# Kernel tuning notes

Measured on AMD Instinct MI355X. Metric: run time of the kernel, lower is better.

The kernel has to match this reference:

```python
import jax, jax.numpy as jnp
import numpy as np

B, H, T, D = 2, 16, 2048, 64


def setup_inputs() -> dict:
    key = jax.random.key(0)
    kq, kk, kv, km = jax.random.split(key, 4)
    q = jax.random.normal(kq, (B, H, T, D), dtype=jnp.float32)
    k = jax.random.normal(kk, (B, H, T, D), dtype=jnp.float32)
    v = jax.random.normal(kv, (B, H, T, D), dtype=jnp.float32)
    mask = jax.random.randint(km, (T, T), 0, 2, dtype=jnp.int32)
    return {"q": q, "k": k, "v": v, "mask": mask}


def reference(q, k, v, mask):
    d_k = q.shape[-1]
    scale = jnp.asarray(d_k, q.dtype) ** -0.5
    # (B,H,T,D) @ (B,H,D,T) -> (B,H,T,T)
    scores = jnp.einsum("bhtd,bhsd->bhts", q * scale, k)
    # mask broadcast over (B,H); masked positions set to -1e9 as in torch code
    scores = jnp.where(mask[None, None, :, :] == 0, jnp.asarray(-1e9, scores.dtype), scores)
    attn = jax.nn.softmax(scores, axis=-1)
    # (B,H,T,T) @ (B,H,T,D) -> (B,H,T,D)
    out = jnp.einsum("bhts,bhsd->bhtd", attn, v)
    return (out, attn)
```

## Files before the change

kernel.cpp:

```cpp
#include <hip/hip_runtime.h>
#include <hip/hip_bf16.h>
#include <cstddef>

#define T_SEQ 2048
#define D_HEAD 64
#define BC 64
#define NKT (T_SEQ / BC)
#define PAD 72

typedef __bf16 bf16x8 __attribute__((ext_vector_type(8)));
typedef float f32x4 __attribute__((ext_vector_type(4)));
typedef unsigned short u16x8 __attribute__((ext_vector_type(8)));

__device__ __forceinline__ unsigned short f2bf(float f) {
  __bf16 h = (__bf16)f;
  return __builtin_bit_cast(unsigned short, h);
}
__device__ __forceinline__ bf16x8 ldfrag(const unsigned short* p) {
  u16x8 t = *(const u16x8*)p;
  return __builtin_bit_cast(bf16x8, t);
}
__device__ __forceinline__ f32x4 mfma16(bf16x8 a, bf16x8 b, f32x4 c) {
  return __builtin_amdgcn_mfma_f32_16x16x32_bf16(a, b, c, 0, 0, 0);
}
__device__ __forceinline__ void bar_sync() {
  asm volatile("" ::: "memory");
  __builtin_amdgcn_s_barrier();
  asm volatile("" ::: "memory");
}
__device__ __forceinline__ void lds_fence() {
  asm volatile("s_waitcnt lgkmcnt(0)" ::: "memory");
}
__device__ __forceinline__ float exp2_hw(float x) { return __builtin_amdgcn_exp2f(x); }
__device__ __forceinline__ float log2_hw(float x) { return __builtin_amdgcn_logf(x); }

__global__ __launch_bounds__(256) void mask_pack(const int* __restrict__ maskg,
                                                 unsigned* __restrict__ mp) {
  const size_t total = (size_t)T_SEQ * T_SEQ;
  size_t idx = (size_t)blockIdx.x * blockDim.x + threadIdx.x;
  const size_t stride = (size_t)gridDim.x * blockDim.x;
  const int lane = threadIdx.x & 63;
  for (; idx < total; idx += stride) {
    int mv = maskg[idx];
    unsigned long long b = __ballot(mv != 0);
    if (lane == 0)       mp[idx >> 5] = (unsigned)b;
    else if (lane == 32) mp[idx >> 5] = (unsigned)(b >> 32);
  }
}

__global__ __launch_bounds__(256, 5) void attn_fused2(
    const float* __restrict__ qg, const float* __restrict__ kg,
    const float* __restrict__ vg, const unsigned* __restrict__ mpk,
    float* __restrict__ outg, float* __restrict__ attng)
{
  __shared__ unsigned short ks[BC][PAD];
  __shared__ unsigned short vt[D_HEAD][PAD];
  __shared__ unsigned short ps[64][PAD];

  const int bid = blockIdx.x;
  const int lin = (bid & 7) * 128 + (bid >> 3);
  const int bh  = lin >> 5;
  const int strip = lin & 31;

  const int tid  = threadIdx.x;
  const int lane = tid & 63;
  const int wid  = tid >> 6;
  const int lr = lane & 15, lh = lane >> 4;
  const int r0 = strip * 64 + wid * 16;
  const int sv = tid >> 2;
  const int sc4 = (tid & 3) << 4;
  const int vt7 = tid & 7;
  const int vs2 = (tid >> 3) * 2;

  const float C = 0.18033688011112042f;
  const float* qb = qg + (size_t)bh * T_SEQ * D_HEAD;
  const float* kb = kg + (size_t)bh * T_SEQ * D_HEAD;
  const float* vb = vg + (size_t)bh * T_SEQ * D_HEAD;
  const int ROWW = T_SEQ / 32;

  bf16x8 qf[2];
  {
    const float* qr = qb + (size_t)(r0 + lr) * D_HEAD;
    #pragma unroll
    for (int kk = 0; kk < 2; ++kk) {
      float4 a = *(const float4*)(qr + kk * 32 + lh * 8);
      float4 b = *(const float4*)(qr + kk * 32 + lh * 8 + 4);
      u16x8 u;
      u[0] = f2bf(a.x); u[1] = f2bf(a.y); u[2] = f2bf(a.z); u[3] = f2bf(a.w);
      u[4] = f2bf(b.x); u[5] = f2bf(b.y); u[6] = f2bf(b.z); u[7] = f2bf(b.w);
      qf[kk] = __builtin_bit_cast(bf16x8, u);
    }
  }

  const f32x4 zero4 = {0.f, 0.f, 0.f, 0.f};
  f32x4 acc[4];
  #pragma unroll
  for (int nt = 0; nt < 4; ++nt) acc[nt] = zero4;
  float psum_s = 0.f;

  for (int kt = 0; kt < NKT; ++kt) {
    const int n0 = kt * BC;
    bar_sync();
    {
      const float* ksrc = kb + (size_t)(n0 + sv) * D_HEAD + sc4;
      float4 k0 = *(const float4*)(ksrc + 0),  k1 = *(const float4*)(ksrc + 4);
      float4 k2 = *(const float4*)(ksrc + 8),  k3 = *(const float4*)(ksrc + 12);
      *(ushort4*)&ks[sv][sc4 + 0]  = make_ushort4(f2bf(k0.x), f2bf(k0.y), f2bf(k0.z), f2bf(k0.w));
      *(ushort4*)&ks[sv][sc4 + 4]  = make_ushort4(f2bf(k1.x), f2bf(k1.y), f2bf(k1.z), f2bf(k1.w));
      *(ushort4*)&ks[sv][sc4 + 8]  = make_ushort4(f2bf(k2.x), f2bf(k2.y), f2bf(k2.z), f2bf(k2.w));
      *(ushort4*)&ks[sv][sc4 + 12] = make_ushort4(f2bf(k3.x), f2bf(k3.y), f2bf(k3.z), f2bf(k3.w));
    }
    {
      const float* v0 = vb + (size_t)(n0 + vs2) * D_HEAD + vt7;
      const float* v1 = v0 + D_HEAD;
      #pragma unroll
      for (int j = 0; j < 8; ++j) {
        const float a = v0[8 * j];
        const float b = v1[8 * j];
        const unsigned w = (unsigned)f2bf(a) | ((unsigned)f2bf(b) << 16);
        *(unsigned*)&vt[vt7 + 8 * j][vs2] = w;
      }
    }
    const unsigned mw0 = mpk[(size_t)(r0 + lr) * ROWW + kt * 2];
    const unsigned mw1 = mpk[(size_t)(r0 + lr) * ROWW + kt * 2 + 1];
    lds_fence(); bar_sync();

    f32x4 st[4];
    #pragma unroll
    for (int nt = 0; nt < 4; ++nt) st[nt] = zero4;
    #pragma unroll
    for (int kk = 0; kk < 2; ++kk) {
      bf16x8 kf[4];
      #pragma unroll
      for (int nt = 0; nt < 4; ++nt) kf[nt] = ldfrag(&ks[nt * 16 + lr][kk * 32 + lh * 8]);
      #pragma unroll
      for (int nt = 0; nt < 4; ++nt) st[nt] = mfma16(kf[nt], qf[kk], st[nt]);
    }
    #pragma unroll
    for (int nt = 0; nt < 4; ++nt) {
      const unsigned w = (nt & 2) ? mw1 : mw0;
      float p[4];
      #pragma unroll
      for (int r = 0; r < 4; ++r) {
        const int bit = (nt & 1) * 16 + 4 * lh + r;
        p[r] = ((w >> bit) & 1) ? exp2_hw(st[nt][r] * C) : 0.f;
        psum_s += p[r];
      }
      const unsigned w0 = (unsigned)f2bf(p[0]) | ((unsigned)f2bf(p[1]) << 16);
      const unsigned w1 = (unsigned)f2bf(p[2]) | ((unsigned)f2bf(p[3]) << 16);
      *(unsigned*)&ps[wid * 16 + lr][nt * 16 + 4 * lh]     = w0;
      *(unsigned*)&ps[wid * 16 + lr][nt * 16 + 4 * lh + 2] = w1;
    }
    lds_fence();
    #pragma unroll
    for (int kk = 0; kk < 2; ++kk) {
      const bf16x8 pa = ldfrag(&ps[wid * 16 + lr][kk * 32 + lh * 8]);
      #pragma unroll
      for (int nt = 0; nt < 4; ++nt) {
        const bf16x8 vf = ldfrag(&vt[nt * 16 + lr][kk * 32 + lh * 8]);
        acc[nt] = mfma16(pa, vf, acc[nt]);
      }
    }
  }

  {
    psum_s += __shfl_xor(psum_s, 16);
    psum_s += __shfl_xor(psum_s, 32);
  }
  const float iv_s = 1.0f / psum_s;
  float ivq[4], lg2ivq[4];
  #pragma unroll
  for (int r = 0; r < 4; ++r) {
    ivq[r] = __shfl(iv_s, 4 * lh + r);
    lg2ivq[r] = log2_hw(ivq[r]);
  }

  float* ob = outg + (size_t)(bh * T_SEQ + r0) * D_HEAD;
  #pragma unroll
  for (int nt = 0; nt < 4; ++nt)
    #pragma unroll
    for (int r = 0; r < 4; ++r)
      ob[(size_t)(4 * lh + r) * D_HEAD + nt * 16 + lr] = acc[nt][r] * ivq[r];

  float* ab = attng + (size_t)(bh * T_SEQ + r0) * T_SEQ;
  for (int kt = 0; kt < NKT; ++kt) {
    const int n0 = kt * BC;
    bar_sync();
    {
      const float* ksrc = kb + (size_t)(n0 + sv) * D_HEAD + sc4;
      float4 k0 = *(const float4*)(ksrc + 0),  k1 = *(const float4*)(ksrc + 4);
      float4 k2 = *(const float4*)(ksrc + 8),  k3 = *(const float4*)(ksrc + 12);
      *(ushort4*)&ks[sv][sc4 + 0]  = make_ushort4(f2bf(k0.x), f2bf(k0.y), f2bf(k0.z), f2bf(k0.w));
      *(ushort4*)&ks[sv][sc4 + 4]  = make_ushort4(f2bf(k1.x), f2bf(k1.y), f2bf(k1.z), f2bf(k1.w));
      *(ushort4*)&ks[sv][sc4 + 8]  = make_ushort4(f2bf(k2.x), f2bf(k2.y), f2bf(k2.z), f2bf(k2.w));
      *(ushort4*)&ks[sv][sc4 + 12] = make_ushort4(f2bf(k3.x), f2bf(k3.y), f2bf(k3.z), f2bf(k3.w));
    }
    unsigned mw[4][2];
    #pragma unroll
    for (int r = 0; r < 4; ++r) {
      const size_t mrow = (size_t)(r0 + 4 * lh + r) * ROWW + kt * 2;
      mw[r][0] = mpk[mrow];
      mw[r][1] = mpk[mrow + 1];
    }
    lds_fence(); bar_sync();

    f32x4 sc_[4];
    #pragma unroll
    for (int nt = 0; nt < 4; ++nt) sc_[nt] = zero4;
    #pragma unroll
    for (int kk = 0; kk < 2; ++kk) {
      bf16x8 kf[4];
      #pragma unroll
      for (int nt = 0; nt < 4; ++nt) kf[nt] = ldfrag(&ks[nt * 16 + lr][kk * 32 + lh * 8]);
      #pragma unroll
      for (int nt = 0; nt < 4; ++nt) sc_[nt] = mfma16(qf[kk], kf[nt], sc_[nt]);
    }
    #pragma unroll
    for (int r = 0; r < 4; ++r) {
      float* arow = ab + (size_t)(4 * lh + r) * T_SEQ + n0;
      #pragma unroll
      for (int nt = 0; nt < 4; ++nt) {
        const int mv = (mw[r][nt >> 1] >> ((nt & 1) * 16 + lr)) & 1;
        const float p = mv ? exp2_hw(__builtin_fmaf(sc_[nt][r], C, lg2ivq[r])) : 0.f;
        __builtin_nontemporal_store(p, arow + nt * 16 + lr);
      }
    }
  }
}

__global__ __launch_bounds__(512, 2) void attn_fused_fb(
    const float* __restrict__ qg, const float* __restrict__ kg,
    const float* __restrict__ vg, const int* __restrict__ maskg,
    float* __restrict__ outg, float* __restrict__ attng)
{
  __shared__ unsigned short qs[128][PAD];
  __shared__ unsigned short ks[64][PAD];
  __shared__ unsigned short vt[64][PAD];
  __shared__ unsigned short pp[128][PAD];
  __shared__ float rsum[128];
  int bid = blockIdx.x;
  int lin = (bid & 7) * 64 + (bid >> 3);
  int bh = lin >> 4, br0 = (lin & 15) * 128;
  const int tid = threadIdx.x, lane = tid & 63, wid = tid >> 6;
  const int wm = wid >> 1, wn = wid & 1, lr = lane & 15, lh = lane >> 4;
  const float scale = 0.125f;
  const float* qb = qg + ((size_t)bh * T_SEQ + br0) * D_HEAD;
  const float* kbp = kg + (size_t)bh * T_SEQ * D_HEAD;
  const float* vbp = vg + (size_t)bh * T_SEQ * D_HEAD;
  if (tid < 128) rsum[tid] = 0.f;
  #pragma unroll
  for (int it = 0; it < 4; ++it) {
    int idx = it * 512 + tid;
    int r = idx >> 4, c = (idx & 15) << 2;
    float4 f = *(const float4*)(qb + (size_t)r * D_HEAD + c);
    *(ushort4*)&qs[r][c] = make_ushort4(f2bf(f.x), f2bf(f.y), f2bf(f.z), f2bf(f.w));
  }
  f32x4 acc_o[2][2];
  const f32x4 zero4 = {0.f, 0.f, 0.f, 0.f};
  #pragma unroll
  for (int a = 0; a < 2; ++a)
    #pragma unroll
    for (int b = 0; b < 2; ++b) acc_o[a][b] = zero4;
  float psum[2][4] = {{0.f,0.f,0.f,0.f},{0.f,0.f,0.f,0.f}};
  __syncthreads();
  for (int kt = 0; kt < NKT; ++kt) {
    const int kb0 = kt * 64;
    #pragma unroll
    for (int it = 0; it < 2; ++it) {
      int idx = it * 512 + tid;
      int r = idx >> 4, c = (idx & 15) << 2;
      float4 f = *(const float4*)(kbp + (size_t)(kb0 + r) * D_HEAD + c);
      *(ushort4*)&ks[r][c] = make_ushort4(f2bf(f.x), f2bf(f.y), f2bf(f.z), f2bf(f.w));
      float4 g = *(const float4*)(vbp + (size_t)(kb0 + r) * D_HEAD + c);
      vt[c+0][r] = f2bf(g.x); vt[c+1][r] = f2bf(g.y);
      vt[c+2][r] = f2bf(g.z); vt[c+3][r] = f2bf(g.w);
    }
    __syncthreads();
    f32x4 sc[2][2];
    #pragma unroll
// ... 78 lines not shown
      int idx = it * 512 + tid;
      int r = idx >> 4, c = (idx & 15) << 2;
      float4 f = *(const float4*)(kbp + (size_t)(kb0 + r) * D_HEAD + c);
      *(ushort4*)&ks[r][c] = make_ushort4(f2bf(f.x), f2bf(f.y), f2bf(f.z), f2bf(f.w));
    }
    __syncthreads();
    f32x4 sc[2][2];
    #pragma unroll
    for (int a = 0; a < 2; ++a)
      #pragma unroll
      for (int b = 0; b < 2; ++b) sc[a][b] = zero4;
    #pragma unroll
    for (int kk = 0; kk < 2; ++kk) {
      const int ke = kk * 32 + lh * 8;
      bf16x8 af[2], bfq[2];
      #pragma unroll
      for (int mt = 0; mt < 2; ++mt) af[mt] = ldfrag(&qs[wm*32 + mt*16 + lr][ke]);
      #pragma unroll
      for (int nt = 0; nt < 2; ++nt) bfq[nt] = ldfrag(&ks[wn*32 + nt*16 + lr][ke]);
      #pragma unroll
      for (int mt = 0; mt < 2; ++mt)
        #pragma unroll
        for (int nt = 0; nt < 2; ++nt)
          sc[mt][nt] = mfma16(af[mt], bfq[nt], sc[mt][nt]);
    }
    #pragma unroll
    for (int mt = 0; mt < 2; ++mt)
      #pragma unroll
      for (int nt = 0; nt < 2; ++nt)
        #pragma unroll
        for (int r = 0; r < 4; ++r) {
          int row = wm*32 + mt*16 + lh*4 + r, col = wn*32 + nt*16 + lr;
          int mv = maskg[(size_t)(br0 + row) * T_SEQ + (kb0 + col)];
          float p = mv ? __expf(sc[mt][nt][r] * scale) * invs[mt][r] : 0.f;
          ab[(size_t)row * T_SEQ + kb0 + col] = p;
        }
  }
}

extern "C" void kernel_launch(void* const* d_in, const int* in_sizes, int n_in,
                              void* d_out, int out_size, void* d_ws, size_t ws_size,
                              hipStream_t stream) {
  const float* q = (const float*)d_in[0];
  const float* k = (const float*)d_in[1];
  const float* v = (const float*)d_in[2];
  const int* mask = (const int*)d_in[3];
  float* out = (float*)d_out;
  float* attn = out + (size_t)2 * 16 * T_SEQ * D_HEAD;

  const size_t mpk_bytes = (size_t)T_SEQ * T_SEQ / 8;
  if (ws_size >= mpk_bytes) {
    unsigned* mp = (unsigned*)d_ws;
    mask_pack<<<dim3(2048), 256, 0, stream>>>(mask, mp);
    attn_fused2<<<dim3(1024), 256, 0, stream>>>(q, k, v, mp, out, attn);
  } else {
    attn_fused_fb<<<dim3(512), 512, 0, stream>>>(q, k, v, mask, out, attn);
  }
}
```

Before: 190.4 us.

## Process two row strips per block, fusing strip-A attn write with strip-B PV pass

Each block now handles two 64-row strips, and the grid is halved. The second sweep over K/V does two jobs at once: it computes strip B's softmax sums and PV accumulation, and it writes the normalized attention for strip A. This saves one full K staging pass per pair of strips, since there are now three sweeps per two strips instead of four. The cost is more registers (launch bounds drop from 5 to 4 blocks per CU) and only 512 blocks, which gives less parallelism across the GPU.

```diff
diff --git a/kernel.cpp b/kernel.cpp
--- a/kernel.cpp
+++ b/kernel.cpp
@@ -48,7 +48,7 @@
   }
 }
 
-__global__ __launch_bounds__(256, 5) void attn_fused2(
+__global__ __launch_bounds__(256, 4) void attn_fused3(
     const float* __restrict__ qg, const float* __restrict__ kg,
     const float* __restrict__ vg, const unsigned* __restrict__ mpk,
     float* __restrict__ outg, float* __restrict__ attng)
@@ -58,15 +58,16 @@
   __shared__ unsigned short ps[64][PAD];
 
   const int bid = blockIdx.x;
-  const int lin = (bid & 7) * 128 + (bid >> 3);
-  const int bh  = lin >> 5;
-  const int strip = lin & 31;
+  const int lin = (bid & 7) * 64 + (bid >> 3);
+  const int bh  = lin >> 4;
+  const int pair = lin & 15;
 
   const int tid  = threadIdx.x;
   const int lane = tid & 63;
   const int wid  = tid >> 6;
   const int lr = lane & 15, lh = lane >> 4;
-  const int r0 = strip * 64 + wid * 16;
+  const int r0A = pair * 128 + wid * 16;
+  const int r0B = r0A + 64;
   const int sv = tid >> 2;
   const int sc4 = (tid & 3) << 4;
   const int vt7 = tid & 7;
@@ -77,10 +78,12 @@
   const float* kb = kg + (size_t)bh * T_SEQ * D_HEAD;
   const float* vb = vg + (size_t)bh * T_SEQ * D_HEAD;
   const int ROWW = T_SEQ / 32;
-
-  bf16x8 qf[2];
-  {
-    const float* qr = qb + (size_t)(r0 + lr) * D_HEAD;
+  const f32x4 zero4 = {0.f, 0.f, 0.f, 0.f};
+
+  bf16x8 qfA[2], qfB[2];
+  #pragma unroll
+  for (int s = 0; s < 2; ++s) {
+    const float* qr = qb + (size_t)((s ? r0B : r0A) + lr) * D_HEAD;
     #pragma unroll
     for (int kk = 0; kk < 2; ++kk) {
       float4 a = *(const float4*)(qr + kk * 32 + lh * 8);
@@ -88,11 +91,37 @@
       u16x8 u;
       u[0] = f2bf(a.x); u[1] = f2bf(a.y); u[2] = f2bf(a.z); u[3] = f2bf(a.w);
       u[4] = f2bf(b.x); u[5] = f2bf(b.y); u[6] = f2bf(b.z); u[7] = f2bf(b.w);
-      qf[kk] = __builtin_bit_cast(bf16x8, u);
-    }
-  }
-
-  const f32x4 zero4 = {0.f, 0.f, 0.f, 0.f};
+      if (s) qfB[kk] = __builtin_bit_cast(bf16x8, u);
+      else   qfA[kk] = __builtin_bit_cast(bf16x8, u);
+    }
+  }
+
+  auto stageKV = [&](int n0) {
+    const float* ksrc = kb + (size_t)(n0 + sv) * D_HEAD + sc4;
+    float4 k0 = *(const float4*)(ksrc + 0),  k1 = *(const float4*)(ksrc + 4);
+    float4 k2 = *(const float4*)(ksrc + 8),  k3 = *(const float4*)(ksrc + 12);
+    *(ushort4*)&ks[sv][sc4 + 0]  = make_ushort4(f2bf(k0.x), f2bf(k0.y), f2bf(k0.z), f2bf(k0.w));
+    *(ushort4*)&ks[sv][sc4 + 4]  = make_ushort4(f2bf(k1.x), f2bf(k1.y), f2bf(k1.z), f2bf(k1.w));
+    *(ushort4*)&ks[sv][sc4 + 8]  = make_ushort4(f2bf(k2.x), f2bf(k2.y), f2bf(k2.z), f2bf(k2.w));
+    *(ushort4*)&ks[sv][sc4 + 12] = make_ushort4(f2bf(k3.x), f2bf(k3.y), f2bf(k3.z), f2bf(k3.w));
+    const float* v0 = vb + (size_t)(n0 + vs2) * D_HEAD + vt7;
+    const float* v1 = v0 + D_HEAD;
+    #pragma unroll
+    for (int j = 0; j < 8; ++j) {
+      const unsigned w = (unsigned)f2bf(v0[8 * j]) | ((unsigned)f2bf(v1[8 * j]) << 16);
+      *(unsigned*)&vt[vt7 + 8 * j][vs2] = w;
+    }
+  };
+  auto stageK = [&](int n0) {
+    const float* ksrc = kb + (size_t)(n0 + sv) * D_HEAD + sc4;
+    float4 k0 = *(const float4*)(ksrc + 0),  k1 = *(const float4*)(ksrc + 4);
+    float4 k2 = *(const float4*)(ksrc + 8),  k3 = *(const float4*)(ksrc + 12);
+    *(ushort4*)&ks[sv][sc4 + 0]  = make_ushort4(f2bf(k0.x), f2bf(k0.y), f2bf(k0.z), f2bf(k0.w));
+    *(ushort4*)&ks[sv][sc4 + 4]  = make_ushort4(f2bf(k1.x), f2bf(k1.y), f2bf(k1.z), f2bf(k1.w));
+    *(ushort4*)&ks[sv][sc4 + 8]  = make_ushort4(f2bf(k2.x), f2bf(k2.y), f2bf(k2.z), f2bf(k2.w));
+    *(ushort4*)&ks[sv][sc4 + 12] = make_ushort4(f2bf(k3.x), f2bf(k3.y), f2bf(k3.z), f2bf(k3.w));
+  };
+
   f32x4 acc[4];
   #pragma unroll
   for (int nt = 0; nt < 4; ++nt) acc[nt] = zero4;
@@ -101,28 +130,9 @@
   for (int kt = 0; kt < NKT; ++kt) {
     const int n0 = kt * BC;
     bar_sync();
-    {
-      const float* ksrc = kb + (size_t)(n0 + sv) * D_HEAD + sc4;
-      float4 k0 = *(const float4*)(ksrc + 0),  k1 = *(const float4*)(ksrc + 4);
-      float4 k2 = *(const float4*)(ksrc + 8),  k3 = *(const float4*)(ksrc + 12);
-      *(ushort4*)&ks[sv][sc4 + 0]  = make_ushort4(f2bf(k0.x), f2bf(k0.y), f2bf(k0.z), f2bf(k0.w));
-      *(ushort4*)&ks[sv][sc4 + 4]  = make_ushort4(f2bf(k1.x), f2bf(k1.y), f2bf(k1.z), f2bf(k1.w));
-      *(ushort4*)&ks[sv][sc4 + 8]  = make_ushort4(f2bf(k2.x), f2bf(k2.y), f2bf(k2.z), f2bf(k2.w));
-      *(ushort4*)&ks[sv][sc4 + 12] = make_ushort4(f2bf(k3.x), f2bf(k3.y), f2bf(k3.z), f2bf(k3.w));
-    }
-    {
-      const float* v0 = vb + (size_t)(n0 + vs2) * D_HEAD + vt7;
-      const float* v1 = v0 + D_HEAD;
-      #pragma unroll
-      for (int j = 0; j < 8; ++j) {
-        const float a = v0[8 * j];
-        const float b = v1[8 * j];
-        const unsigned w = (unsigned)f2bf(a) | ((unsigned)f2bf(b) << 16);
-        *(unsigned*)&vt[vt7 + 8 * j][vs2] = w;
-      }
-    }
-    const unsigned mw0 = mpk[(size_t)(r0 + lr) * ROWW + kt * 2];
-    const unsigned mw1 = mpk[(size_t)(r0 + lr) * ROWW + kt * 2 + 1];
+    stageKV(n0);
+    const unsigned mw0 = mpk[(size_t)(r0A + lr) * ROWW + kt * 2];
+    const unsigned mw1 = mpk[(size_t)(r0A + lr) * ROWW + kt * 2 + 1];
     lds_fence(); bar_sync();
 
     f32x4 st[4];
@@ -134,7 +144,7 @@
       #pragma unroll
       for (int nt = 0; nt < 4; ++nt) kf[nt] = ldfrag(&ks[nt * 16 + lr][kk * 32 + lh * 8]);
       #pragma unroll
-      for (int nt = 0; nt < 4; ++nt) st[nt] = mfma16(kf[nt], qf[kk], st[nt]);
+      for (int nt = 0; nt < 4; ++nt) st[nt] = mfma16(kf[nt], qfA[kk], st[nt]);
     }
     #pragma unroll
     for (int nt = 0; nt < 4; ++nt) {
@@ -146,59 +156,131 @@
         p[r] = ((w >> bit) & 1) ? exp2_hw(st[nt][r] * C) : 0.f;
         psum_s += p[r];
       }
-      const unsigned w0 = (unsigned)f2bf(p[0]) | ((unsigned)f2bf(p[1]) << 16);
-      const unsigned w1 = (unsigned)f2bf(p[2]) | ((unsigned)f2bf(p[3]) << 16);
-      *(unsigned*)&ps[wid * 16 + lr][nt * 16 + 4 * lh]     = w0;
-      *(unsigned*)&ps[wid * 16 + lr][nt * 16 + 4 * lh + 2] = w1;
+      *(unsigned*)&ps[wid * 16 + lr][nt * 16 + 4 * lh]     = (unsigned)f2bf(p[0]) | ((unsigned)f2bf(p[1]) << 16);
+      *(unsigned*)&ps[wid * 16 + lr][nt * 16 + 4 * lh + 2] = (unsigned)f2bf(p[2]) | ((unsigned)f2bf(p[3]) << 16);
     }
     lds_fence();
     #pragma unroll
     for (int kk = 0; kk < 2; ++kk) {
       const bf16x8 pa = ldfrag(&ps[wid * 16 + lr][kk * 32 + lh * 8]);
       #pragma unroll
-      for (int nt = 0; nt < 4; ++nt) {
-        const bf16x8 vf = ldfrag(&vt[nt * 16 + lr][kk * 32 + lh * 8]);
-        acc[nt] = mfma16(pa, vf, acc[nt]);
-      }
-    }
-  }
-
+      for (int nt = 0; nt < 4; ++nt)
+        acc[nt] = mfma16(pa, ldfrag(&vt[nt * 16 + lr][kk * 32 + lh * 8]), acc[nt]);
+    }
+  }
+
+  psum_s += __shfl_xor(psum_s, 16);
+  psum_s += __shfl_xor(psum_s, 32);
+  const float ivA_s = 1.0f / psum_s;
+  float ivqA[4], lgA[4];
+  #pragma unroll
+  for (int r = 0; r < 4; ++r) {
+    ivqA[r] = __shfl(ivA_s, 4 * lh + r);
+    lgA[r] = log2_hw(ivqA[r]);
+  }
   {
-    psum_s += __shfl_xor(psum_s, 16);
-    psum_s += __shfl_xor(psum_s, 32);
-  }
-  const float iv_s = 1.0f / psum_s;
-  float ivq[4], lg2ivq[4];
-  #pragma unroll
-  for (int r = 0; r < 4; ++r) {
-    ivq[r] = __shfl(iv_s, 4 * lh + r);
-    lg2ivq[r] = log2_hw(ivq[r]);
-  }
-
-  float* ob = outg + (size_t)(bh * T_SEQ + r0) * D_HEAD;
-  #pragma unroll
-  for (int nt = 0; nt < 4; ++nt)
-    #pragma unroll
-    for (int r = 0; r < 4; ++r)
-      ob[(size_t)(4 * lh + r) * D_HEAD + nt * 16 + lr] = acc[nt][r] * ivq[r];
-
-  float* ab = attng + (size_t)(bh * T_SEQ + r0) * T_SEQ;
+    float* ob = outg + (size_t)(bh * T_SEQ + r0A) * D_HEAD;
+    #pragma unroll
+    for (int nt = 0; nt < 4; ++nt)
+      #pragma unroll
+      for (int r = 0; r < 4; ++r)
+        ob[(size_t)(4 * lh + r) * D_HEAD + nt * 16 + lr] = acc[nt][r] * ivqA[r];
+  }
+
+  #pragma unroll
+  for (int nt = 0; nt < 4; ++nt) acc[nt] = zero4;
+  psum_s = 0.f;
+  float* abA = attng + (size_t)(bh * T_SEQ + r0A) * T_SEQ;
+
   for (int kt = 0; kt < NKT; ++kt) {
     const int n0 = kt * BC;
     bar_sync();
-    {
-      const float* ksrc = kb + (size_t)(n0 + sv) * D_HEAD + sc4;
-      float4 k0 = *(const float4*)(ksrc + 0),  k1 = *(const float4*)(ksrc + 4);
-      float4 k2 = *(const float4*)(ksrc + 8),  k3 = *(const float4*)(ksrc + 12);
-      *(ushort4*)&ks[sv][sc4 + 0]  = make_ushort4(f2bf(k0.x), f2bf(k0.y), f2bf(k0.z), f2bf(k0.w));
-      *(ushort4*)&ks[sv][sc4 + 4]  = make_ushort4(f2bf(k1.x), f2bf(k1.y), f2bf(k1.z), f2bf(k1.w));
-      *(ushort4*)&ks[sv][sc4 + 8]  = make_ushort4(f2bf(k2.x), f2bf(k2.y), f2bf(k2.z), f2bf(k2.w));
-      *(ushort4*)&ks[sv][sc4 + 12] = make_ushort4(f2bf(k3.x), f2bf(k3.y), f2bf(k3.z), f2bf(k3.w));
-    }
+    stageKV(n0);
+    const unsigned mwB0 = mpk[(size_t)(r0B + lr) * ROWW + kt * 2];
+    const unsigned mwB1 = mpk[(size_t)(r0B + lr) * ROWW + kt * 2 + 1];
+    unsigned mwA[4][2];
+    #pragma unroll
+    for (int r = 0; r < 4; ++r) {
+      const size_t mrow = (size_t)(r0A + 4 * lh + r) * ROWW + kt * 2;
+      mwA[r][0] = mpk[mrow];
+      mwA[r][1] = mpk[mrow + 1];
+    }
+    lds_fence(); bar_sync();
+
+    f32x4 stB[4], scA[4];
+    #pragma unroll
+    for (int nt = 0; nt < 4; ++nt) { stB[nt] = zero4; scA[nt] = zero4; }
+    #pragma unroll
+    for (int kk = 0; kk < 2; ++kk) {
+      bf16x8 kf[4];
+      #pragma unroll
+      for (int nt = 0; nt < 4; ++nt) kf[nt] = ldfrag(&ks[nt * 16 + lr][kk * 32 + lh * 8]);
+      #pragma unroll
+      for (int nt = 0; nt < 4; ++nt) {
+        stB[nt] = mfma16(kf[nt], qfB[kk], stB[nt]);
+        scA[nt] = mfma16(qfA[kk], kf[nt], scA[nt]);
+      }
+    }
+    #pragma unroll
+    for (int nt = 0; nt < 4; ++nt) {
+      const unsigned w = (nt & 2) ? mwB1 : mwB0;
+      float p[4];
+      #pragma unroll
+      for (int r = 0; r < 4; ++r) {
+        const int bit = (nt & 1) * 16 + 4 * lh + r;
+        p[r] = ((w >> bit) & 1) ? exp2_hw(stB[nt][r] * C) : 0.f;
+        psum_s += p[r];
+      }
+      *(unsigned*)&ps[wid * 16 + lr][nt * 16 + 4 * lh]     = (unsigned)f2bf(p[0]) | ((unsigned)f2bf(p[1]) << 16);
+      *(unsigned*)&ps[wid * 16 + lr][nt * 16 + 4 * lh + 2] = (unsigned)f2bf(p[2]) | ((unsigned)f2bf(p[3]) << 16);
+    }
+    #pragma unroll
+    for (int r = 0; r < 4; ++r) {
+      float* arow = abA + (size_t)(4 * lh + r) * T_SEQ + n0;
+      #pragma unroll
+      for (int nt = 0; nt < 4; ++nt) {
+        const int mv = (mwA[r][nt >> 1] >> ((nt & 1) * 16 + lr)) & 1;
+        const float p = mv ? exp2_hw(__builtin_fmaf(scA[nt][r], C, lgA[r])) : 0.f;
+        __builtin_nontemporal_store(p, arow + nt * 16 + lr);
+      }
+    }
+    lds_fence();
+    #pragma unroll
+    for (int kk = 0; kk < 2; ++kk) {
+      const bf16x8 pa = ldfrag(&ps[wid * 16 + lr][kk * 32 + lh * 8]);
+      #pragma unroll
+      for (int nt = 0; nt < 4; ++nt)
+        acc[nt] = mfma16(pa, ldfrag(&vt[nt * 16 + lr][kk * 32 + lh * 8]), acc[nt]);
+    }
+  }
+
+  psum_s += __shfl_xor(psum_s, 16);
+  psum_s += __shfl_xor(psum_s, 32);
+  const float ivB_s = 1.0f / psum_s;
+  float ivqB[4], lgB[4];
+  #pragma unroll
+  for (int r = 0; r < 4; ++r) {
+    ivqB[r] = __shfl(ivB_s, 4 * lh + r);
+    lgB[r] = log2_hw(ivqB[r]);
+  }
+  {
+    float* ob = outg + (size_t)(bh * T_SEQ + r0B) * D_HEAD;
+    #pragma unroll
+    for (int nt = 0; nt < 4; ++nt)
+      #pragma unroll
+      for (int r = 0; r < 4; ++r)
+        ob[(size_t)(4 * lh + r) * D_HEAD + nt * 16 + lr] = acc[nt][r] * ivqB[r];
+  }
+
+  float* abB = attng + (size_t)(bh * T_SEQ + r0B) * T_SEQ;
+  for (int kt = 0; kt < NKT; ++kt) {
+    const int n0 = kt * BC;
+    bar_sync();
+    stageK(n0);
     unsigned mw[4][2];
     #pragma unroll
     for (int r = 0; r < 4; ++r) {
-      const size_t mrow = (size_t)(r0 + 4 * lh + r) * ROWW + kt * 2;
+      const size_t mrow = (size_t)(r0B + 4 * lh + r) * ROWW + kt * 2;
       mw[r][0] = mpk[mrow];
       mw[r][1] = mpk[mrow + 1];
     }
@@ -213,15 +295,15 @@
       #pragma unroll
       for (int nt = 0; nt < 4; ++nt) kf[nt] = ldfrag(&ks[nt * 16 + lr][kk * 32 + lh * 8]);
       #pragma unroll
-      for (int nt = 0; nt < 4; ++nt) sc_[nt] = mfma16(qf[kk], kf[nt], sc_[nt]);
+      for (int nt = 0; nt < 4; ++nt) sc_[nt] = mfma16(qfB[kk], kf[nt], sc_[nt]);
     }
     #pragma unroll
     for (int r = 0; r < 4; ++r) {
-      float* arow = ab + (size_t)(4 * lh + r) * T_SEQ + n0;
+      float* arow = abB + (size_t)(4 * lh + r) * T_SEQ + n0;
       #pragma unroll
       for (int nt = 0; nt < 4; ++nt) {
         const int mv = (mw[r][nt >> 1] >> ((nt & 1) * 16 + lr)) & 1;
-        const float p = mv ? exp2_hw(__builtin_fmaf(sc_[nt][r], C, lg2ivq[r])) : 0.f;
+        const float p = mv ? exp2_hw(__builtin_fmaf(sc_[nt][r], C, lgB[r])) : 0.f;
         __builtin_nontemporal_store(p, arow + nt * 16 + lr);
       }
     }
@@ -409,7 +491,7 @@
   if (ws_size >= mpk_bytes) {
     unsigned* mp = (unsigned*)d_ws;
     mask_pack<<<dim3(2048), 256, 0, stream>>>(mask, mp);
-    attn_fused2<<<dim3(1024), 256, 0, stream>>>(q, k, v, mp, out, attn);
+    attn_fused3<<<dim3(512), 256, 0, stream>>>(q, k, v, mp, out, attn);
   } else {
     attn_fused_fb<<<dim3(512), 512, 0, stream>>>(q, k, v, mask, out, attn);
   }
```

Result: slower. 223.1 us (+17.2%).

## Prefetch next K/V tile and mask words into registers during compute

Applied to the files above, without the earlier changes.

Both passes of the fused attention kernel now issue global loads for the next K (and V) tile and the next mask words before the current tile's MFMA work. The loaded values are written to shared memory only after a barrier at the end of the iteration. This hides global-load latency behind compute and the attn stores, at the cost of more live registers, so the launch-bounds occupancy hint drops from 5 to 4 blocks. The added sched_barrier keeps the compiler from sinking the prefetch loads.

```diff
diff --git a/kernel.cpp b/kernel.cpp
--- a/kernel.cpp
+++ b/kernel.cpp
@@ -48,7 +48,7 @@
   }
 }
 
-__global__ __launch_bounds__(256, 5) void attn_fused2(
+__global__ __launch_bounds__(256, 4) void attn_fused4(
     const float* __restrict__ qg, const float* __restrict__ kg,
     const float* __restrict__ vg, const unsigned* __restrict__ mpk,
     float* __restrict__ outg, float* __restrict__ attng)
@@ -77,6 +77,7 @@
   const float* kb = kg + (size_t)bh * T_SEQ * D_HEAD;
   const float* vb = vg + (size_t)bh * T_SEQ * D_HEAD;
   const int ROWW = T_SEQ / 32;
+  const f32x4 zero4 = {0.f, 0.f, 0.f, 0.f};
 
   bf16x8 qf[2];
   {
@@ -92,38 +93,53 @@
     }
   }
 
-  const f32x4 zero4 = {0.f, 0.f, 0.f, 0.f};
   f32x4 acc[4];
   #pragma unroll
   for (int nt = 0; nt < 4; ++nt) acc[nt] = zero4;
   float psum_s = 0.f;
 
+  {
+    const float* ksrc = kb + (size_t)sv * D_HEAD + sc4;
+    float4 k0 = *(const float4*)(ksrc + 0),  k1 = *(const float4*)(ksrc + 4);
+    float4 k2 = *(const float4*)(ksrc + 8),  k3 = *(const float4*)(ksrc + 12);
+    *(ushort4*)&ks[sv][sc4 + 0]  = make_ushort4(f2bf(k0.x), f2bf(k0.y), f2bf(k0.z), f2bf(k0.w));
+    *(ushort4*)&ks[sv][sc4 + 4]  = make_ushort4(f2bf(k1.x), f2bf(k1.y), f2bf(k1.z), f2bf(k1.w));
+    *(ushort4*)&ks[sv][sc4 + 8]  = make_ushort4(f2bf(k2.x), f2bf(k2.y), f2bf(k2.z), f2bf(k2.w));
+    *(ushort4*)&ks[sv][sc4 + 12] = make_ushort4(f2bf(k3.x), f2bf(k3.y), f2bf(k3.z), f2bf(k3.w));
+    const float* v0p = vb + (size_t)vs2 * D_HEAD + vt7;
+    const float* v1p = v0p + D_HEAD;
+    #pragma unroll
+    for (int j = 0; j < 8; ++j) {
+      const unsigned w = (unsigned)f2bf(v0p[8 * j]) | ((unsigned)f2bf(v1p[8 * j]) << 16);
+      *(unsigned*)&vt[vt7 + 8 * j][vs2] = w;
+    }
+  }
+  unsigned cm0 = mpk[(size_t)(r0 + lr) * ROWW + 0];
+  unsigned cm1 = mpk[(size_t)(r0 + lr) * ROWW + 1];
+  lds_fence(); bar_sync();
+
   for (int kt = 0; kt < NKT; ++kt) {
-    const int n0 = kt * BC;
-    bar_sync();
+    const int kn  = (kt + 1 < NKT) ? kt + 1 : kt;
+    const int nn0 = kn * BC;
+
+    float4 pk[4];
     {
-      const float* ksrc = kb + (size_t)(n0 + sv) * D_HEAD + sc4;
-      float4 k0 = *(const float4*)(ksrc + 0),  k1 = *(const float4*)(ksrc + 4);
-      float4 k2 = *(const float4*)(ksrc + 8),  k3 = *(const float4*)(ksrc + 12);
-      *(ushort4*)&ks[sv][sc4 + 0]  = make_ushort4(f2bf(k0.x), f2bf(k0.y), f2bf(k0.z), f2bf(k0.w));
-      *(ushort4*)&ks[sv][sc4 + 4]  = make_ushort4(f2bf(k1.x), f2bf(k1.y), f2bf(k1.z), f2bf(k1.w));
-      *(ushort4*)&ks[sv][sc4 + 8]  = make_ushort4(f2bf(k2.x), f2bf(k2.y), f2bf(k2.z), f2bf(k2.w));
-      *(ushort4*)&ks[sv][sc4 + 12] = make_ushort4(f2bf(k3.x), f2bf(k3.y), f2bf(k3.z), f2bf(k3.w));
-    }
+      const float* ksrc = kb + (size_t)(nn0 + sv) * D_HEAD + sc4;
+      pk[0] = *(const float4*)(ksrc + 0);
+      pk[1] = *(const float4*)(ksrc + 4);
+      pk[2] = *(const float4*)(ksrc + 8);
+      pk[3] = *(const float4*)(ksrc + 12);
+    }
+    float pva[8], pvb[8];
     {
-      const float* v0 = vb + (size_t)(n0 + vs2) * D_HEAD + vt7;
-      const float* v1 = v0 + D_HEAD;
-      #pragma unroll
-      for (int j = 0; j < 8; ++j) {
-        const float a = v0[8 * j];
-        const float b = v1[8 * j];
-        const unsigned w = (unsigned)f2bf(a) | ((unsigned)f2bf(b) << 16);
-        *(unsigned*)&vt[vt7 + 8 * j][vs2] = w;
-      }
-    }
-    const unsigned mw0 = mpk[(size_t)(r0 + lr) * ROWW + kt * 2];
-    const unsigned mw1 = mpk[(size_t)(r0 + lr) * ROWW + kt * 2 + 1];
-    lds_fence(); bar_sync();
+      const float* v0p = vb + (size_t)(nn0 + vs2) * D_HEAD + vt7;
+      const float* v1p = v0p + D_HEAD;
+      #pragma unroll
+      for (int j = 0; j < 8; ++j) { pva[j] = v0p[8 * j]; pvb[j] = v1p[8 * j]; }
+    }
+    const unsigned nm0 = mpk[(size_t)(r0 + lr) * ROWW + kn * 2];
+    const unsigned nm1 = mpk[(size_t)(r0 + lr) * ROWW + kn * 2 + 1];
+    __builtin_amdgcn_sched_barrier(0);
 
     f32x4 st[4];
     #pragma unroll
@@ -138,7 +154,7 @@
     }
     #pragma unroll
     for (int nt = 0; nt < 4; ++nt) {
-      const unsigned w = (nt & 2) ? mw1 : mw0;
+      const unsigned w = (nt & 2) ? cm1 : cm0;
       float p[4];
       #pragma unroll
       for (int r = 0; r < 4; ++r) {
@@ -146,27 +162,34 @@
         p[r] = ((w >> bit) & 1) ? exp2_hw(st[nt][r] * C) : 0.f;
         psum_s += p[r];
       }
-      const unsigned w0 = (unsigned)f2bf(p[0]) | ((unsigned)f2bf(p[1]) << 16);
-      const unsigned w1 = (unsigned)f2bf(p[2]) | ((unsigned)f2bf(p[3]) << 16);
-      *(unsigned*)&ps[wid * 16 + lr][nt * 16 + 4 * lh]     = w0;
-      *(unsigned*)&ps[wid * 16 + lr][nt * 16 + 4 * lh + 2] = w1;
+      *(unsigned*)&ps[wid * 16 + lr][nt * 16 + 4 * lh]     = (unsigned)f2bf(p[0]) | ((unsigned)f2bf(p[1]) << 16);
+      *(unsigned*)&ps[wid * 16 + lr][nt * 16 + 4 * lh + 2] = (unsigned)f2bf(p[2]) | ((unsigned)f2bf(p[3]) << 16);
     }
     lds_fence();
     #pragma unroll
     for (int kk = 0; kk < 2; ++kk) {
       const bf16x8 pa = ldfrag(&ps[wid * 16 + lr][kk * 32 + lh * 8]);
       #pragma unroll
-      for (int nt = 0; nt < 4; ++nt) {
-        const bf16x8 vf = ldfrag(&vt[nt * 16 + lr][kk * 32 + lh * 8]);
-        acc[nt] = mfma16(pa, vf, acc[nt]);
-      }
-    }
-  }
-
-  {
-    psum_s += __shfl_xor(psum_s, 16);
-    psum_s += __shfl_xor(psum_s, 32);
-  }
+      for (int nt = 0; nt < 4; ++nt)
+        acc[nt] = mfma16(pa, ldfrag(&vt[nt * 16 + lr][kk * 32 + lh * 8]), acc[nt]);
+    }
+
+    bar_sync();
+    *(ushort4*)&ks[sv][sc4 + 0]  = make_ushort4(f2bf(pk[0].x), f2bf(pk[0].y), f2bf(pk[0].z), f2bf(pk[0].w));
+    *(ushort4*)&ks[sv][sc4 + 4]  = make_ushort4(f2bf(pk[1].x), f2bf(pk[1].y), f2bf(pk[1].z), f2bf(pk[1].w));
+    *(ushort4*)&ks[sv][sc4 + 8]  = make_ushort4(f2bf(pk[2].x), f2bf(pk[2].y), f2bf(pk[2].z), f2bf(pk[2].w));
+    *(ushort4*)&ks[sv][sc4 + 12] = make_ushort4(f2bf(pk[3].x), f2bf(pk[3].y), f2bf(pk[3].z), f2bf(pk[3].w));
+    #pragma unroll
+    for (int j = 0; j < 8; ++j) {
+      const unsigned w = (unsigned)f2bf(pva[j]) | ((unsigned)f2bf(pvb[j]) << 16);
+      *(unsigned*)&vt[vt7 + 8 * j][vs2] = w;
+    }
+    lds_fence(); bar_sync();
+    cm0 = nm0; cm1 = nm1;
+  }
+
+  psum_s += __shfl_xor(psum_s, 16);
+  psum_s += __shfl_xor(psum_s, 32);
   const float iv_s = 1.0f / psum_s;
   float ivq[4], lg2ivq[4];
   #pragma unroll
@@ -182,27 +205,46 @@
     for (int r = 0; r < 4; ++r)
       ob[(size_t)(4 * lh + r) * D_HEAD + nt * 16 + lr] = acc[nt][r] * ivq[r];
 
+  {
+    const float* ksrc = kb + (size_t)sv * D_HEAD + sc4;
+    float4 k0 = *(const float4*)(ksrc + 0),  k1 = *(const float4*)(ksrc + 4);
+    float4 k2 = *(const float4*)(ksrc + 8),  k3 = *(const float4*)(ksrc + 12);
+    *(ushort4*)&ks[sv][sc4 + 0]  = make_ushort4(f2bf(k0.x), f2bf(k0.y), f2bf(k0.z), f2bf(k0.w));
+    *(ushort4*)&ks[sv][sc4 + 4]  = make_ushort4(f2bf(k1.x), f2bf(k1.y), f2bf(k1.z), f2bf(k1.w));
+    *(ushort4*)&ks[sv][sc4 + 8]  = make_ushort4(f2bf(k2.x), f2bf(k2.y), f2bf(k2.z), f2bf(k2.w));
+    *(ushort4*)&ks[sv][sc4 + 12] = make_ushort4(f2bf(k3.x), f2bf(k3.y), f2bf(k3.z), f2bf(k3.w));
+  }
+  unsigned m2[4][2];
+  #pragma unroll
+  for (int r = 0; r < 4; ++r) {
+    const size_t mrow = (size_t)(r0 + 4 * lh + r) * ROWW;
+    m2[r][0] = mpk[mrow];
+    m2[r][1] = mpk[mrow + 1];
+  }
+  lds_fence(); bar_sync();
+
   float* ab = attng + (size_t)(bh * T_SEQ + r0) * T_SEQ;
   for (int kt = 0; kt < NKT; ++kt) {
-    const int n0 = kt * BC;
-    bar_sync();
+    const int n0  = kt * BC;
+    const int kn  = (kt + 1 < NKT) ? kt + 1 : kt;
+    const int nn0 = kn * BC;
+
+    float4 pk[4];
     {
-      const float* ksrc = kb + (size_t)(n0 + sv) * D_HEAD + sc4;
-      float4 k0 = *(const float4*)(ksrc + 0),  k1 = *(const float4*)(ksrc + 4);
-      float4 k2 = *(const float4*)(ksrc + 8),  k3 = *(const float4*)(ksrc + 12);
-      *(ushort4*)&ks[sv][sc4 + 0]  = make_ushort4(f2bf(k0.x), f2bf(k0.y), f2bf(k0.z), f2bf(k0.w));
-      *(ushort4*)&ks[sv][sc4 + 4]  = make_ushort4(f2bf(k1.x), f2bf(k1.y), f2bf(k1.z), f2bf(k1.w));
-      *(ushort4*)&ks[sv][sc4 + 8]  = make_ushort4(f2bf(k2.x), f2bf(k2.y), f2bf(k2.z), f2bf(k2.w));
-      *(ushort4*)&ks[sv][sc4 + 12] = make_ushort4(f2bf(k3.x), f2bf(k3.y), f2bf(k3.z), f2bf(k3.w));
-    }
-    unsigned mw[4][2];
+      const float* ksrc = kb + (size_t)(nn0 + sv) * D_HEAD + sc4;
+      pk[0] = *(const float4*)(ksrc + 0);
+      pk[1] = *(const float4*)(ksrc + 4);
+      pk[2] = *(const float4*)(ksrc + 8);
+      pk[3] = *(const float4*)(ksrc + 12);
+    }
+    unsigned nm2[4][2];
     #pragma unroll
     for (int r = 0; r < 4; ++r) {
-      const size_t mrow = (size_t)(r0 + 4 * lh + r) * ROWW + kt * 2;
-      mw[r][0] = mpk[mrow];
-      mw[r][1] = mpk[mrow + 1];
-    }
-    lds_fence(); bar_sync();
+      const size_t mrow = (size_t)(r0 + 4 * lh + r) * ROWW + kn * 2;
+      nm2[r][0] = mpk[mrow];
+      nm2[r][1] = mpk[mrow + 1];
+    }
+    __builtin_amdgcn_sched_barrier(0);
 
     f32x4 sc_[4];
     #pragma unroll
@@ -220,11 +262,20 @@
       float* arow = ab + (size_t)(4 * lh + r) * T_SEQ + n0;
       #pragma unroll
       for (int nt = 0; nt < 4; ++nt) {
-        const int mv = (mw[r][nt >> 1] >> ((nt & 1) * 16 + lr)) & 1;
+        const int mv = (m2[r][nt >> 1] >> ((nt & 1) * 16 + lr)) & 1;
         const float p = mv ? exp2_hw(__builtin_fmaf(sc_[nt][r], C, lg2ivq[r])) : 0.f;
         __builtin_nontemporal_store(p, arow + nt * 16 + lr);
       }
     }
+
+    bar_sync();
+    *(ushort4*)&ks[sv][sc4 + 0]  = make_ushort4(f2bf(pk[0].x), f2bf(pk[0].y), f2bf(pk[0].z), f2bf(pk[0].w));
+    *(ushort4*)&ks[sv][sc4 + 4]  = make_ushort4(f2bf(pk[1].x), f2bf(pk[1].y), f2bf(pk[1].z), f2bf(pk[1].w));
+    *(ushort4*)&ks[sv][sc4 + 8]  = make_ushort4(f2bf(pk[2].x), f2bf(pk[2].y), f2bf(pk[2].z), f2bf(pk[2].w));
+    *(ushort4*)&ks[sv][sc4 + 12] = make_ushort4(f2bf(pk[3].x), f2bf(pk[3].y), f2bf(pk[3].z), f2bf(pk[3].w));
+    lds_fence(); bar_sync();
+    #pragma unroll
+    for (int r = 0; r < 4; ++r) { m2[r][0] = nm2[r][0]; m2[r][1] = nm2[r][1]; }
   }
 }
 
@@ -409,7 +460,7 @@
   if (ws_size >= mpk_bytes) {
     unsigned* mp = (unsigned*)d_ws;
     mask_pack<<<dim3(2048), 256, 0, stream>>>(mask, mp);
-    attn_fused2<<<dim3(1024), 256, 0, stream>>>(q, k, v, mp, out, attn);
+    attn_fused4<<<dim3(1024), 256, 0, stream>>>(q, k, v, mp, out, attn);
   } else {
     attn_fused_fb<<<dim3(512), 512, 0, stream>>>(q, k, v, mask, out, attn);
   }
```

Measured after the change: 226.9 us. 1.19x slower.

## Halve block threads, give each wave two 16-row query strips

Applied to the files above, without the earlier changes.

The attention kernel now launches 128 threads (2 waves) per block instead of 256. Each wave processes two 16-row query strips, so every K/V fragment read from LDS feeds two MFMAs. The K and V staging loops cover the 64-row tile in two passes and use wider 16-byte LDS stores. The aim is to cut LDS fragment traffic per MFMA and raise instruction-level parallelism, at the cost of more registers per thread and fewer waves available to hide load latency.

```diff
diff --git a/kernel.cpp b/kernel.cpp
--- a/kernel.cpp
+++ b/kernel.cpp
@@ -7,6 +7,7 @@
 #define BC 64
 #define NKT (T_SEQ / BC)
 #define PAD 72
+#define NTHR 128
 
 typedef __bf16 bf16x8 __attribute__((ext_vector_type(8)));
 typedef float f32x4 __attribute__((ext_vector_type(4)));
@@ -48,7 +49,7 @@
   }
 }
 
-__global__ __launch_bounds__(256, 5) void attn_fused2(
+__global__ __launch_bounds__(NTHR, 2) void attn_fused5(
     const float* __restrict__ qg, const float* __restrict__ kg,
     const float* __restrict__ vg, const unsigned* __restrict__ mpk,
     float* __restrict__ outg, float* __restrict__ attng)
@@ -60,13 +61,14 @@
   const int bid = blockIdx.x;
   const int lin = (bid & 7) * 128 + (bid >> 3);
   const int bh  = lin >> 5;
-  const int strip = lin & 31;
+  const int blk64 = (lin & 31) * 64;
 
   const int tid  = threadIdx.x;
   const int lane = tid & 63;
   const int wid  = tid >> 6;
   const int lr = lane & 15, lh = lane >> 4;
-  const int r0 = strip * 64 + wid * 16;
+  const int r0s0 = blk64 + wid * 32;
+  const int r0s1 = r0s0 + 16;
   const int sv = tid >> 2;
   const int sc4 = (tid & 3) << 4;
   const int vt7 = tid & 7;
@@ -77,10 +79,12 @@
   const float* kb = kg + (size_t)bh * T_SEQ * D_HEAD;
   const float* vb = vg + (size_t)bh * T_SEQ * D_HEAD;
   const int ROWW = T_SEQ / 32;
-
-  bf16x8 qf[2];
-  {
-    const float* qr = qb + (size_t)(r0 + lr) * D_HEAD;
+  const f32x4 zero4 = {0.f, 0.f, 0.f, 0.f};
+
+  bf16x8 qf[2][2];
+  #pragma unroll
+  for (int s = 0; s < 2; ++s) {
+    const float* qr = qb + (size_t)((s ? r0s1 : r0s0) + lr) * D_HEAD;
     #pragma unroll
     for (int kk = 0; kk < 2; ++kk) {
       float4 a = *(const float4*)(qr + kk * 32 + lh * 8);
@@ -88,141 +92,177 @@
       u16x8 u;
       u[0] = f2bf(a.x); u[1] = f2bf(a.y); u[2] = f2bf(a.z); u[3] = f2bf(a.w);
       u[4] = f2bf(b.x); u[5] = f2bf(b.y); u[6] = f2bf(b.z); u[7] = f2bf(b.w);
-      qf[kk] = __builtin_bit_cast(bf16x8, u);
-    }
-  }
-
-  const f32x4 zero4 = {0.f, 0.f, 0.f, 0.f};
-  f32x4 acc[4];
-  #pragma unroll
-  for (int nt = 0; nt < 4; ++nt) acc[nt] = zero4;
-  float psum_s = 0.f;
+      qf[s][kk] = __builtin_bit_cast(bf16x8, u);
+    }
+  }
+
+  f32x4 acc[2][4];
+  #pragma unroll
+  for (int s = 0; s < 2; ++s)
+    #pragma unroll
+    for (int nt = 0; nt < 4; ++nt) acc[s][nt] = zero4;
+  float psum[2] = {0.f, 0.f};
 
   for (int kt = 0; kt < NKT; ++kt) {
     const int n0 = kt * BC;
     bar_sync();
-    {
-      const float* ksrc = kb + (size_t)(n0 + sv) * D_HEAD + sc4;
+    #pragma unroll
+    for (int it = 0; it < 2; ++it) {
+      const int row = sv + it * 32;
+      const float* ksrc = kb + (size_t)(n0 + row) * D_HEAD + sc4;
       float4 k0 = *(const float4*)(ksrc + 0),  k1 = *(const float4*)(ksrc + 4);
       float4 k2 = *(const float4*)(ksrc + 8),  k3 = *(const float4*)(ksrc + 12);
-      *(ushort4*)&ks[sv][sc4 + 0]  = make_ushort4(f2bf(k0.x), f2bf(k0.y), f2bf(k0.z), f2bf(k0.w));
-      *(ushort4*)&ks[sv][sc4 + 4]  = make_ushort4(f2bf(k1.x), f2bf(k1.y), f2bf(k1.z), f2bf(k1.w));
-      *(ushort4*)&ks[sv][sc4 + 8]  = make_ushort4(f2bf(k2.x), f2bf(k2.y), f2bf(k2.z), f2bf(k2.w));
-      *(ushort4*)&ks[sv][sc4 + 12] = make_ushort4(f2bf(k3.x), f2bf(k3.y), f2bf(k3.z), f2bf(k3.w));
-    }
-    {
-      const float* v0 = vb + (size_t)(n0 + vs2) * D_HEAD + vt7;
-      const float* v1 = v0 + D_HEAD;
+      u16x8 w0, w1;
+      w0[0]=f2bf(k0.x); w0[1]=f2bf(k0.y); w0[2]=f2bf(k0.z); w0[3]=f2bf(k0.w);
+      w0[4]=f2bf(k1.x); w0[5]=f2bf(k1.y); w0[6]=f2bf(k1.z); w0[7]=f2bf(k1.w);
+      w1[0]=f2bf(k2.x); w1[1]=f2bf(k2.y); w1[2]=f2bf(k2.z); w1[3]=f2bf(k2.w);
+      w1[4]=f2bf(k3.x); w1[5]=f2bf(k3.y); w1[6]=f2bf(k3.z); w1[7]=f2bf(k3.w);
+      *(u16x8*)&ks[row][sc4 + 0] = w0;
+      *(u16x8*)&ks[row][sc4 + 8] = w1;
+      const int s0 = vs2 + it * 32;
+      const float* v0p = vb + (size_t)(n0 + s0) * D_HEAD + vt7;
+      const float* v1p = v0p + D_HEAD;
       #pragma unroll
       for (int j = 0; j < 8; ++j) {
-        const float a = v0[8 * j];
-        const float b = v1[8 * j];
-        const unsigned w = (unsigned)f2bf(a) | ((unsigned)f2bf(b) << 16);
-        *(unsigned*)&vt[vt7 + 8 * j][vs2] = w;
-      }
-    }
-    const unsigned mw0 = mpk[(size_t)(r0 + lr) * ROWW + kt * 2];
-    const unsigned mw1 = mpk[(size_t)(r0 + lr) * ROWW + kt * 2 + 1];
+        const unsigned w = (unsigned)f2bf(v0p[8 * j]) | ((unsigned)f2bf(v1p[8 * j]) << 16);
+        *(unsigned*)&vt[vt7 + 8 * j][s0] = w;
+      }
+    }
+    const unsigned m00 = mpk[(size_t)(r0s0 + lr) * ROWW + kt * 2];
+    const unsigned m01 = mpk[(size_t)(r0s0 + lr) * ROWW + kt * 2 + 1];
+    const unsigned m10 = mpk[(size_t)(r0s1 + lr) * ROWW + kt * 2];
+    const unsigned m11 = mpk[(size_t)(r0s1 + lr) * ROWW + kt * 2 + 1];
     lds_fence(); bar_sync();
 
-    f32x4 st[4];
-    #pragma unroll
-    for (int nt = 0; nt < 4; ++nt) st[nt] = zero4;
+    f32x4 st[2][4];
+    #pragma unroll
+    for (int s = 0; s < 2; ++s)
+      #pragma unroll
+      for (int nt = 0; nt < 4; ++nt) st[s][nt] = zero4;
     #pragma unroll
     for (int kk = 0; kk < 2; ++kk) {
       bf16x8 kf[4];
       #pragma unroll
       for (int nt = 0; nt < 4; ++nt) kf[nt] = ldfrag(&ks[nt * 16 + lr][kk * 32 + lh * 8]);
       #pragma unroll
-      for (int nt = 0; nt < 4; ++nt) st[nt] = mfma16(kf[nt], qf[kk], st[nt]);
-    }
-    #pragma unroll
-    for (int nt = 0; nt < 4; ++nt) {
-      const unsigned w = (nt & 2) ? mw1 : mw0;
-      float p[4];
-      #pragma unroll
-      for (int r = 0; r < 4; ++r) {
-        const int bit = (nt & 1) * 16 + 4 * lh + r;
-        p[r] = ((w >> bit) & 1) ? exp2_hw(st[nt][r] * C) : 0.f;
-        psum_s += p[r];
-      }
-      const unsigned w0 = (unsigned)f2bf(p[0]) | ((unsigned)f2bf(p[1]) << 16);
-      const unsigned w1 = (unsigned)f2bf(p[2]) | ((unsigned)f2bf(p[3]) << 16);
-      *(unsigned*)&ps[wid * 16 + lr][nt * 16 + 4 * lh]     = w0;
-      *(unsigned*)&ps[wid * 16 + lr][nt * 16 + 4 * lh + 2] = w1;
+      for (int nt = 0; nt < 4; ++nt) {
+        st[0][nt] = mfma16(kf[nt], qf[0][kk], st[0][nt]);
+        st[1][nt] = mfma16(kf[nt], qf[1][kk], st[1][nt]);
+      }
+    }
+    #pragma unroll
+    for (int s = 0; s < 2; ++s) {
+      const unsigned w0m = s ? m10 : m00;
+      const unsigned w1m = s ? m11 : m01;
+      #pragma unroll
+      for (int nt = 0; nt < 4; ++nt) {
+        const unsigned w = (nt & 2) ? w1m : w0m;
+        float p[4];
+        #pragma unroll
+        for (int r = 0; r < 4; ++r) {
+          const int bit = (nt & 1) * 16 + 4 * lh + r;
+          p[r] = ((w >> bit) & 1) ? exp2_hw(st[s][nt][r] * C) : 0.f;
+          psum[s] += p[r];
+        }
+        uint2 u;
+        u.x = (unsigned)f2bf(p[0]) | ((unsigned)f2bf(p[1]) << 16);
+        u.y = (unsigned)f2bf(p[2]) | ((unsigned)f2bf(p[3]) << 16);
+        *(uint2*)&ps[wid * 32 + s * 16 + lr][nt * 16 + 4 * lh] = u;
+      }
     }
     lds_fence();
     #pragma unroll
     for (int kk = 0; kk < 2; ++kk) {
-      const bf16x8 pa = ldfrag(&ps[wid * 16 + lr][kk * 32 + lh * 8]);
+      const bf16x8 pa0 = ldfrag(&ps[wid * 32 + lr][kk * 32 + lh * 8]);
+      const bf16x8 pa1 = ldfrag(&ps[wid * 32 + 16 + lr][kk * 32 + lh * 8]);
       #pragma unroll
       for (int nt = 0; nt < 4; ++nt) {
         const bf16x8 vf = ldfrag(&vt[nt * 16 + lr][kk * 32 + lh * 8]);
-        acc[nt] = mfma16(pa, vf, acc[nt]);
-      }
-    }
-  }
-
-  {
-    psum_s += __shfl_xor(psum_s, 16);
-    psum_s += __shfl_xor(psum_s, 32);
-  }
-  const float iv_s = 1.0f / psum_s;
-  float ivq[4], lg2ivq[4];
-  #pragma unroll
-  for (int r = 0; r < 4; ++r) {
-    ivq[r] = __shfl(iv_s, 4 * lh + r);
-    lg2ivq[r] = log2_hw(ivq[r]);
-  }
-
-  float* ob = outg + (size_t)(bh * T_SEQ + r0) * D_HEAD;
-  #pragma unroll
-  for (int nt = 0; nt < 4; ++nt)
-    #pragma unroll
-    for (int r = 0; r < 4; ++r)
-      ob[(size_t)(4 * lh + r) * D_HEAD + nt * 16 + lr] = acc[nt][r] * ivq[r];
-
-  float* ab = attng + (size_t)(bh * T_SEQ + r0) * T_SEQ;
+        acc[0][nt] = mfma16(pa0, vf, acc[0][nt]);
+        acc[1][nt] = mfma16(pa1, vf, acc[1][nt]);
+      }
+    }
+  }
+
+  float lg2ivq[2][4];
+  #pragma unroll
+  for (int s = 0; s < 2; ++s) {
+    float ssum = psum[s];
+    ssum += __shfl_xor(ssum, 16);
+    ssum += __shfl_xor(ssum, 32);
+    const float iv_s = 1.0f / ssum;
+    float ivq[4];
+    #pragma unroll
+    for (int r = 0; r < 4; ++r) {
+      ivq[r] = __shfl(iv_s, 4 * lh + r);
+      lg2ivq[s][r] = log2_hw(ivq[r]);
+    }
+    float* ob = outg + (size_t)(bh * T_SEQ + (s ? r0s1 : r0s0)) * D_HEAD;
+    #pragma unroll
+    for (int nt = 0; nt < 4; ++nt)
+      #pragma unroll
+      for (int r = 0; r < 4; ++r)
+        ob[(size_t)(4 * lh + r) * D_HEAD + nt * 16 + lr] = acc[s][nt][r] * ivq[r];
+  }
+
+  float* ab0 = attng + (size_t)(bh * T_SEQ + r0s0) * T_SEQ;
+  float* ab1 = attng + (size_t)(bh * T_SEQ + r0s1) * T_SEQ;
   for (int kt = 0; kt < NKT; ++kt) {
     const int n0 = kt * BC;
     bar_sync();
-    {
-      const float* ksrc = kb + (size_t)(n0 + sv) * D_HEAD + sc4;
+    #pragma unroll
+    for (int it = 0; it < 2; ++it) {
+      const int row = sv + it * 32;
+      const float* ksrc = kb + (size_t)(n0 + row) * D_HEAD + sc4;
       float4 k0 = *(const float4*)(ksrc + 0),  k1 = *(const float4*)(ksrc + 4);
       float4 k2 = *(const float4*)(ksrc + 8),  k3 = *(const float4*)(ksrc + 12);
-      *(ushort4*)&ks[sv][sc4 + 0]  = make_ushort4(f2bf(k0.x), f2bf(k0.y), f2bf(k0.z), f2bf(k0.w));
-      *(ushort4*)&ks[sv][sc4 + 4]  = make_ushort4(f2bf(k1.x), f2bf(k1.y), f2bf(k1.z), f2bf(k1.w));
-      *(ushort4*)&ks[sv][sc4 + 8]  = make_ushort4(f2bf(k2.x), f2bf(k2.y), f2bf(k2.z), f2bf(k2.w));
-      *(ushort4*)&ks[sv][sc4 + 12] = make_ushort4(f2bf(k3.x), f2bf(k3.y), f2bf(k3.z), f2bf(k3.w));
-    }
-    unsigned mw[4][2];
-    #pragma unroll
-    for (int r = 0; r < 4; ++r) {
-      const size_t mrow = (size_t)(r0 + 4 * lh + r) * ROWW + kt * 2;
-      mw[r][0] = mpk[mrow];
-      mw[r][1] = mpk[mrow + 1];
-    }
+      u16x8 w0, w1;
+      w0[0]=f2bf(k0.x); w0[1]=f2bf(k0.y); w0[2]=f2bf(k0.z); w0[3]=f2bf(k0.w);
+      w0[4]=f2bf(k1.x); w0[5]=f2bf(k1.y); w0[6]=f2bf(k1.z); w0[7]=f2bf(k1.w);
+      w1[0]=f2bf(k2.x); w1[1]=f2bf(k2.y); w1[2]=f2bf(k2.z); w1[3]=f2bf(k2.w);
+      w1[4]=f2bf(k3.x); w1[5]=f2bf(k3.y); w1[6]=f2bf(k3.z); w1[7]=f2bf(k3.w);
+      *(u16x8*)&ks[row][sc4 + 0] = w0;
+      *(u16x8*)&ks[row][sc4 + 8] = w1;
+    }
+    unsigned mw[2][4][2];
+    #pragma unroll
+    for (int s = 0; s < 2; ++s)
+      #pragma unroll
+      for (int r = 0; r < 4; ++r) {
+        const size_t mrow = (size_t)((s ? r0s1 : r0s0) + 4 * lh + r) * ROWW + kt * 2;
+        mw[s][r][0] = mpk[mrow];
+        mw[s][r][1] = mpk[mrow + 1];
+      }
     lds_fence(); bar_sync();
 
-    f32x4 sc_[4];
-    #pragma unroll
-    for (int nt = 0; nt < 4; ++nt) sc_[nt] = zero4;
+    f32x4 sc_[2][4];
+    #pragma unroll
+    for (int s = 0; s < 2; ++s)
+      #pragma unroll
+      for (int nt = 0; nt < 4; ++nt) sc_[s][nt] = zero4;
     #pragma unroll
     for (int kk = 0; kk < 2; ++kk) {
       bf16x8 kf[4];
       #pragma unroll
       for (int nt = 0; nt < 4; ++nt) kf[nt] = ldfrag(&ks[nt * 16 + lr][kk * 32 + lh * 8]);
       #pragma unroll
-      for (int nt = 0; nt < 4; ++nt) sc_[nt] = mfma16(qf[kk], kf[nt], sc_[nt]);
-    }
-    #pragma unroll
-    for (int r = 0; r < 4; ++r) {
-      float* arow = ab + (size_t)(4 * lh + r) * T_SEQ + n0;
-      #pragma unroll
       for (int nt = 0; nt < 4; ++nt) {
-        const int mv = (mw[r][nt >> 1] >> ((nt & 1) * 16 + lr)) & 1;
-        const float p = mv ? exp2_hw(__builtin_fmaf(sc_[nt][r], C, lg2ivq[r])) : 0.f;
-        __builtin_nontemporal_store(p, arow + nt * 16 + lr);
+        sc_[0][nt] = mfma16(qf[0][kk], kf[nt], sc_[0][nt]);
+        sc_[1][nt] = mfma16(qf[1][kk], kf[nt], sc_[1][nt]);
+      }
+    }
+    #pragma unroll
+    for (int s = 0; s < 2; ++s) {
+      float* ab = s ? ab1 : ab0;
+      #pragma unroll
+      for (int r = 0; r < 4; ++r) {
+        float* arow = ab + (size_t)(4 * lh + r) * T_SEQ + n0;
+        #pragma unroll
+        for (int nt = 0; nt < 4; ++nt) {
+          const int mv = (mw[s][r][nt >> 1] >> ((nt & 1) * 16 + lr)) & 1;
+          const float p = mv ? exp2_hw(__builtin_fmaf(sc_[s][nt][r], C, lg2ivq[s][r])) : 0.f;
+          __builtin_nontemporal_store(p, arow + nt * 16 + lr);
+        }
       }
     }
   }
@@ -409,7 +449,7 @@
   if (ws_size >= mpk_bytes) {
     unsigned* mp = (unsigned*)d_ws;
     mask_pack<<<dim3(2048), 256, 0, stream>>>(mask, mp);
-    attn_fused2<<<dim3(1024), 256, 0, stream>>>(q, k, v, mp, out, attn);
+    attn_fused5<<<dim3(1024), NTHR, 0, stream>>>(q, k, v, mp, out, attn);
   } else {
     attn_fused_fb<<<dim3(512), 512, 0, stream>>>(q, k, v, mask, out, attn);
   }
```

New measurement: 240.9 us. +26.5%, slower.
